# Optimization experiments

Measured on AMD Instinct MI355X. Metric: run time of the kernel, lower is better.

Reference implementation:

```python
import jax, jax.numpy as jnp
import numpy as np
from jax import lax

VOCAB, EMBED, HIDDEN, SEQ = 50257, 1024, 1024, 4096


def setup_inputs() -> dict:
    key = jax.random.key(0)
    ks = jax.random.split(key, 8)
    s = 0.02
    return {
        "input_seq": jax.random.randint(ks[0], (SEQ,), 0, VOCAB),
        "emb": jax.random.normal(ks[1], (VOCAB, EMBED), jnp.float32) * s,
        "Wrx": jax.random.normal(ks[2], (HIDDEN, EMBED), jnp.float32) * s,
        "Wrh": jax.random.normal(ks[3], (HIDDEN, HIDDEN), jnp.float32) * s,
        "Wzx": jax.random.normal(ks[4], (HIDDEN, EMBED), jnp.float32) * s,
        "Wzh": jax.random.normal(ks[5], (HIDDEN, HIDDEN), jnp.float32) * s,
        "Wx": jax.random.normal(ks[6], (HIDDEN, EMBED), jnp.float32) * s,
        "Wh": jax.random.normal(ks[7], (HIDDEN, HIDDEN), jnp.float32) * s,
    }


def reference(input_seq, emb, Wrx, Wrh, Wzx, Wzh, Wx, Wh):
    # Embed whole sequence at once: [S, E]
    x_seq = emb[input_seq]
    # Hoist input-side projections out of the recurrence (one GEMM each): [S, H]
    xr = x_seq @ Wrx.T
    xz = x_seq @ Wzx.T
    xh = x_seq @ Wx.T

    def step(h, xs):
        xr_t, xz_t, xh_t = xs
        z = jax.nn.sigmoid(xz_t + Wzh @ h)          # update gate
        r = jax.nn.sigmoid(xr_t + Wrh @ h)          # reset gate
        h_tilde = jnp.tanh(xh_t + Wh @ (r * h))     # candidate
        h_new = z * h + (1.0 - z) * h_tilde
        return h_new, None

    h0 = jnp.zeros((Wh.shape[0],), dtype=emb.dtype)
    h_final, _ = lax.scan(step, h0, (xr, xz, xh))
    return h_final
```

## Files before the change

kernel.cpp:

```cpp
#include <hip/hip_runtime.h>
#include <stdint.h>


#define HID    1024
#define SEQLEN 4096
#define NWG    64
#define RPW    16
#define BLOCK  512

typedef unsigned long long u64;

__global__ __launch_bounds__(256) void proj_gemm(
    const int* __restrict__ seq, const float* __restrict__ emb,
    const float* __restrict__ Wrx, const float* __restrict__ Wzx,
    const float* __restrict__ Wx,
    float* __restrict__ xr, float* __restrict__ xz, float* __restrict__ xh)
{
  __shared__ float As[32][68];
  __shared__ float Bs[32][68];
  __shared__ int   idx[64];

  const float* W = (blockIdx.z == 0) ? Wrx : (blockIdx.z == 1) ? Wzx : Wx;
  float*       C = (blockIdx.z == 0) ? xr  : (blockIdx.z == 1) ? xz  : xh;

  const int tid = threadIdx.x;
  const int t0 = blockIdx.y * 64;
  const int i0 = blockIdx.x * 64;
  if (tid < 64) idx[tid] = seq[t0 + tid];
  __syncthreads();

  float acc[4][4] = {};
  const int tx = tid & 15, ty = tid >> 4;
  const int c4 = (tid & 7) * 4;
  const int r8 = tid >> 3;

  for (int k0 = 0; k0 < HID; k0 += 32) {
    for (int l = 0; l < 2; ++l) {
      const int rr = r8 + l * 32;
      float4 av = *(const float4*)(emb + (size_t)idx[rr] * HID + k0 + c4);
      As[c4+0][rr]=av.x; As[c4+1][rr]=av.y; As[c4+2][rr]=av.z; As[c4+3][rr]=av.w;
      float4 bv = *(const float4*)(W + (size_t)(i0 + rr) * HID + k0 + c4);
      Bs[c4+0][rr]=bv.x; Bs[c4+1][rr]=bv.y; Bs[c4+2][rr]=bv.z; Bs[c4+3][rr]=bv.w;
    }
    __syncthreads();
    #pragma unroll
    for (int k = 0; k < 32; ++k) {
      float a[4], b[4];
      *(float4*)a = *(const float4*)&As[k][ty * 4];
      *(float4*)b = *(const float4*)&Bs[k][tx * 4];
      #pragma unroll
      for (int i = 0; i < 4; ++i)
        #pragma unroll
        for (int j = 0; j < 4; ++j)
          acc[i][j] = fmaf(a[i], b[j], acc[i][j]);
    }
    __syncthreads();
  }
  #pragma unroll
  for (int i = 0; i < 4; ++i) {
    float4 v = make_float4(acc[i][0], acc[i][1], acc[i][2], acc[i][3]);
    *(float4*)(C + (size_t)(t0 + ty * 4 + i) * HID + i0 + tx * 4) = v;
  }
}

__device__ __forceinline__ void publish2(u64* cells, int row, float a, float b,
                                         unsigned tag) {
  u64 ca = ((u64)tag << 32) | (u64)__float_as_uint(a);
  u64 cb = ((u64)tag << 32) | (u64)__float_as_uint(b);
  (void)__hip_atomic_exchange(&cells[row],     ca, __ATOMIC_RELAXED,
                              __HIP_MEMORY_SCOPE_AGENT);
  (void)__hip_atomic_exchange(&cells[row + 1], cb, __ATOMIC_RELAXED,
                              __HIP_MEMORY_SCOPE_AGENT);
}

__device__ __forceinline__ float2 poll_pair(const u64* cells, int pair,
                                            unsigned want, int* budget) {
  const float* p = (const float*)(cells + 2 * pair);
  float4 v;
  for (;;) {
    asm volatile("global_load_dwordx4 %0, %1, off sc0 sc1\n\ts_waitcnt vmcnt(0)"
                 : "=v"(v) : "v"(p) : "memory");
    if (__float_as_uint(v.y) == want && __float_as_uint(v.w) == want) break;
    if (--(*budget) <= 0) break;
  }
  return make_float2(v.x, v.z);
}

__global__ __launch_bounds__(BLOCK, 2) void rnn_scan(
    const float* __restrict__ Wzh, const float* __restrict__ Wrh,
    const float* __restrict__ Whh,
    const float* __restrict__ xz, const float* __restrict__ xr,
    const float* __restrict__ xh,
    u64* __restrict__ hcell,
    u64* __restrict__ rhcell,
    float* __restrict__ out)
{
  const int tid  = threadIdx.x;
  const int wave = tid >> 6, lane = tid & 63;
  const int g    = blockIdx.x;
  const int rowA = g * RPW + wave * 2;

  __shared__ float h_lds[HID];
  __shared__ float rh_lds[HID];

  float wgt[3][2][16];
  #pragma unroll
  for (int m = 0; m < 3; ++m) {
    const float* Wm = (m == 0) ? Wzh : (m == 1) ? Wrh : Whh;
    #pragma unroll
    for (int rr = 0; rr < 2; ++rr) {
      const float* p = Wm + (size_t)(rowA + rr) * HID + lane * 4;
      #pragma unroll
      for (int q = 0; q < 4; ++q) {
        float4 v = *(const float4*)(p + q * 256);
        wgt[m][rr][q*4+0] = v.x; wgt[m][rr][q*4+1] = v.y;
        wgt[m][rr][q*4+2] = v.z; wgt[m][rr][q*4+3] = v.w;
      }
    }
  }

  int budget = 1 << 21;
  float xzv[2], xrv[2], xhv[2], zv[2], hprev[2];

  for (int t = 1; t <= SEQLEN; ++t) {
    if (t == 1) {
      *(float2*)&h_lds[2 * tid] = make_float2(0.f, 0.f);
    } else {
      float2 hv = poll_pair(hcell + ((t - 1) & 1) * HID, tid,
                            (unsigned)(t - 1), &budget);
      *(float2*)&h_lds[2 * tid] = hv;
    }

    if (lane == 0) {
      #pragma unroll
      for (int rr = 0; rr < 2; ++rr) {
        xzv[rr] = xz[(size_t)(t - 1) * HID + rowA + rr];
        xrv[rr] = xr[(size_t)(t - 1) * HID + rowA + rr];
        xhv[rr] = xh[(size_t)(t - 1) * HID + rowA + rr];
      }
    }
    __syncthreads();

    float hr[16];
    #pragma unroll
    for (int q = 0; q < 4; ++q)
      *(float4*)&hr[q*4] = *(const float4*)&h_lds[q * 256 + lane * 4];
    float az[2] = {0.f, 0.f}, ar[2] = {0.f, 0.f};
    #pragma unroll
    for (int rr = 0; rr < 2; ++rr)
      #pragma unroll
      for (int c = 0; c < 16; ++c) {
        az[rr] = fmaf(wgt[0][rr][c], hr[c], az[rr]);
        ar[rr] = fmaf(wgt[1][rr][c], hr[c], ar[rr]);
      }
    #pragma unroll
    for (int m = 1; m < 64; m <<= 1) {
      az[0] += __shfl_xor(az[0], m, 64);
      az[1] += __shfl_xor(az[1], m, 64);
      ar[0] += __shfl_xor(ar[0], m, 64);
      ar[1] += __shfl_xor(ar[1], m, 64);
    }
    if (lane == 0) {
      float rh[2];
      #pragma unroll
      for (int rr = 0; rr < 2; ++rr) {
        hprev[rr] = h_lds[rowA + rr];
        zv[rr]    = 1.f / (1.f + __expf(-(xzv[rr] + az[rr])));
        float rg  = 1.f / (1.f + __expf(-(xrv[rr] + ar[rr])));
        rh[rr]    = rg * hprev[rr];
      }
      publish2(rhcell + (t & 1) * HID, rowA, rh[0], rh[1], (unsigned)t);
    }

    {
      float2 rv = poll_pair(rhcell + (t & 1) * HID, tid, (unsigned)t, &budget);
      *(float2*)&rh_lds[2 * tid] = rv;
    }
    __syncthreads();

    float rr16[16];
    #pragma unroll
    for (int q = 0; q < 4; ++q)
      *(float4*)&rr16[q*4] = *(const float4*)&rh_lds[q * 256 + lane * 4];
    float ac[2] = {0.f, 0.f};
    #pragma unroll
    for (int rr = 0; rr < 2; ++rr)
      #pragma unroll
      for (int c = 0; c < 16; ++c)
        ac[rr] = fmaf(wgt[2][rr][c], rr16[c], ac[rr]);
    #pragma unroll
    for (int m = 1; m < 64; m <<= 1) {
      ac[0] += __shfl_xor(ac[0], m, 64);
      ac[1] += __shfl_xor(ac[1], m, 64);
    }
    if (lane == 0) {
      float hn[2];
      #pragma unroll
      for (int rr = 0; rr < 2; ++rr) {
        float cand = tanhf(xhv[rr] + ac[rr]);
        hn[rr]     = zv[rr] * hprev[rr] + (1.f - zv[rr]) * cand;
      }
      publish2(hcell + (t & 1) * HID, rowA, hn[0], hn[1], (unsigned)t);
      if (t == SEQLEN) { out[rowA] = hn[0]; out[rowA + 1] = hn[1]; }
    }
  }
}

extern "C" void kernel_launch(void* const* d_in, const int* in_sizes, int n_in,
                              void* d_out, int out_size, void* d_ws, size_t ws_size,
                              hipStream_t stream) {
  (void)in_sizes; (void)n_in; (void)out_size; (void)ws_size;

  const int*   seq = (const int*)d_in[0];
  const float* emb = (const float*)d_in[1];
  const float* Wrx = (const float*)d_in[2];
  const float* Wrh = (const float*)d_in[3];
  const float* Wzx = (const float*)d_in[4];
  const float* Wzh = (const float*)d_in[5];
  const float* Wx  = (const float*)d_in[6];
  const float* Wh  = (const float*)d_in[7];

  char* ws = (char*)d_ws;
  const size_t PROJ = (size_t)SEQLEN * HID * sizeof(float);
  float* xr    = (float*)(ws);
  float* xz    = (float*)(ws + PROJ);
  float* xh    = (float*)(ws + 2 * PROJ);
  u64*   hcell = (u64*)(ws + 3 * PROJ);
  u64*   rhcell= hcell + 2 * HID;

  (void)hipMemsetAsync(hcell, 0xFF, 4 * HID * sizeof(u64), stream);

  proj_gemm<<<dim3(HID / 64, SEQLEN / 64, 3), 256, 0, stream>>>(
      seq, emb, Wrx, Wzx, Wx, xr, xz, xh);

  rnn_scan<<<dim3(NWG), BLOCK, 0, stream>>>(
      Wzh, Wrh, Wh, xz, xr, xh, hcell, rhcell, (float*)d_out);
}
```

Measured before the change: 24.54 ms.

## Replace per-thread tag polling with per-workgroup arrival counters; transpose projections

Each wave now bumps a padded per-workgroup counter after publishing its h or r*h values. Only wave 0 polls those 64 counters before the block does a single tag-checked gather, replacing the old scheme where all 512 threads spun on tagged cells. This is meant to cut polling traffic across the device and the latency of the cross-workgroup barrier. The projection GEMM now writes the xr/xz/xh outputs transposed (row-major per hidden unit), and their per-step loads are issued at the top of each step, ahead of the wait. The cost is extra atomics, a vmcnt wait before each counter bump, and additional block barriers per step.

```diff
diff --git a/kernel.cpp b/kernel.cpp
--- a/kernel.cpp
+++ b/kernel.cpp
@@ -7,6 +7,7 @@
 #define NWG    64
 #define RPW    16
 #define BLOCK  512
+#define SSTR   8
 
 typedef unsigned long long u64;
 
@@ -14,14 +15,14 @@
     const int* __restrict__ seq, const float* __restrict__ emb,
     const float* __restrict__ Wrx, const float* __restrict__ Wzx,
     const float* __restrict__ Wx,
-    float* __restrict__ xr, float* __restrict__ xz, float* __restrict__ xh)
+    float* __restrict__ xrT, float* __restrict__ xzT, float* __restrict__ xhT)
 {
   __shared__ float As[32][68];
   __shared__ float Bs[32][68];
   __shared__ int   idx[64];
 
   const float* W = (blockIdx.z == 0) ? Wrx : (blockIdx.z == 1) ? Wzx : Wx;
-  float*       C = (blockIdx.z == 0) ? xr  : (blockIdx.z == 1) ? xz  : xh;
+  float*       C = (blockIdx.z == 0) ? xrT : (blockIdx.z == 1) ? xzT : xhT;
 
   const int tid = threadIdx.x;
   const int t0 = blockIdx.y * 64;
@@ -46,8 +47,8 @@
     #pragma unroll
     for (int k = 0; k < 32; ++k) {
       float a[4], b[4];
-      *(float4*)a = *(const float4*)&As[k][ty * 4];
-      *(float4*)b = *(const float4*)&Bs[k][tx * 4];
+      *(float4*)a = *(const float4*)&Bs[k][ty * 4];
+      *(float4*)b = *(const float4*)&As[k][tx * 4];
       #pragma unroll
       for (int i = 0; i < 4; ++i)
         #pragma unroll
@@ -59,7 +60,7 @@
   #pragma unroll
   for (int i = 0; i < 4; ++i) {
     float4 v = make_float4(acc[i][0], acc[i][1], acc[i][2], acc[i][3]);
-    *(float4*)(C + (size_t)(t0 + ty * 4 + i) * HID + i0 + tx * 4) = v;
+    *(float4*)(C + (size_t)(i0 + ty * 4 + i) * SEQLEN + t0 + tx * 4) = v;
   }
 }
 
@@ -73,8 +74,8 @@
                               __HIP_MEMORY_SCOPE_AGENT);
 }
 
-__device__ __forceinline__ float2 poll_pair(const u64* cells, int pair,
-                                            unsigned want, int* budget) {
+__device__ __forceinline__ float2 gather_pair(const u64* cells, int pair,
+                                              unsigned want, int* budget) {
   const float* p = (const float*)(cells + 2 * pair);
   float4 v;
   for (;;) {
@@ -86,13 +87,25 @@
   return make_float2(v.x, v.z);
 }
 
+__device__ __forceinline__ void poll_sent(const u64* s, int lane, u64 need,
+                                          int* budget) {
+  const u64* p = s + (size_t)lane * SSTR;
+  for (;;) {
+    u64 v = __hip_atomic_load((u64*)p, __ATOMIC_RELAXED, __HIP_MEMORY_SCOPE_AGENT);
+    if (__all(v >= need)) break;
+    if (--(*budget) <= 0) break;
+  }
+}
+
 __global__ __launch_bounds__(BLOCK, 2) void rnn_scan(
     const float* __restrict__ Wzh, const float* __restrict__ Wrh,
     const float* __restrict__ Whh,
-    const float* __restrict__ xz, const float* __restrict__ xr,
-    const float* __restrict__ xh,
+    const float* __restrict__ xzT, const float* __restrict__ xrT,
+    const float* __restrict__ xhT,
     u64* __restrict__ hcell,
     u64* __restrict__ rhcell,
+    u64* __restrict__ sent_h,
+    u64* __restrict__ sent_rh,
     float* __restrict__ out)
 {
   const int tid  = threadIdx.x;
@@ -123,22 +136,25 @@
   float xzv[2], xrv[2], xhv[2], zv[2], hprev[2];
 
   for (int t = 1; t <= SEQLEN; ++t) {
+    if (lane == 0) {
+      #pragma unroll
+      for (int rr = 0; rr < 2; ++rr) {
+        xzv[rr] = xzT[(size_t)(rowA + rr) * SEQLEN + (t - 1)];
+        xrv[rr] = xrT[(size_t)(rowA + rr) * SEQLEN + (t - 1)];
+        xhv[rr] = xhT[(size_t)(rowA + rr) * SEQLEN + (t - 1)];
+      }
+    }
+
+    float2 hv;
     if (t == 1) {
-      *(float2*)&h_lds[2 * tid] = make_float2(0.f, 0.f);
+      hv = make_float2(0.f, 0.f);
     } else {
-      float2 hv = poll_pair(hcell + ((t - 1) & 1) * HID, tid,
-                            (unsigned)(t - 1), &budget);
-      *(float2*)&h_lds[2 * tid] = hv;
-    }
-
-    if (lane == 0) {
-      #pragma unroll
-      for (int rr = 0; rr < 2; ++rr) {
-        xzv[rr] = xz[(size_t)(t - 1) * HID + rowA + rr];
-        xrv[rr] = xr[(size_t)(t - 1) * HID + rowA + rr];
-        xhv[rr] = xh[(size_t)(t - 1) * HID + rowA + rr];
-      }
-    }
+      if (wave == 0) poll_sent(sent_h, lane, 8ull * (u64)(t - 1), &budget);
+      __syncthreads();
+      hv = gather_pair(hcell + ((t - 1) & 1) * HID, tid,
+                       (unsigned)(t - 1), &budget);
+    }
+    *(float2*)&h_lds[2 * tid] = hv;
     __syncthreads();
 
     float hr[16];
@@ -170,10 +186,15 @@
         rh[rr]    = rg * hprev[rr];
       }
       publish2(rhcell + (t & 1) * HID, rowA, rh[0], rh[1], (unsigned)t);
-    }
-
+      asm volatile("s_waitcnt vmcnt(0)" ::: "memory");
+      (void)__hip_atomic_fetch_add(&sent_rh[(size_t)g * SSTR], 1ull,
+                                   __ATOMIC_RELAXED, __HIP_MEMORY_SCOPE_AGENT);
+    }
+
+    if (wave == 0) poll_sent(sent_rh, lane, 8ull * (u64)t, &budget);
+    __syncthreads();
     {
-      float2 rv = poll_pair(rhcell + (t & 1) * HID, tid, (unsigned)t, &budget);
+      float2 rv = gather_pair(rhcell + (t & 1) * HID, tid, (unsigned)t, &budget);
       *(float2*)&rh_lds[2 * tid] = rv;
     }
     __syncthreads();
@@ -201,6 +222,9 @@
         hn[rr]     = zv[rr] * hprev[rr] + (1.f - zv[rr]) * cand;
       }
       publish2(hcell + (t & 1) * HID, rowA, hn[0], hn[1], (unsigned)t);
+      asm volatile("s_waitcnt vmcnt(0)" ::: "memory");
+      (void)__hip_atomic_fetch_add(&sent_h[(size_t)g * SSTR], 1ull,
+                                   __ATOMIC_RELAXED, __HIP_MEMORY_SCOPE_AGENT);
       if (t == SEQLEN) { out[rowA] = hn[0]; out[rowA + 1] = hn[1]; }
     }
   }
@@ -222,17 +246,21 @@
 
   char* ws = (char*)d_ws;
   const size_t PROJ = (size_t)SEQLEN * HID * sizeof(float);
-  float* xr    = (float*)(ws);
-  float* xz    = (float*)(ws + PROJ);
-  float* xh    = (float*)(ws + 2 * PROJ);
-  u64*   hcell = (u64*)(ws + 3 * PROJ);
-  u64*   rhcell= hcell + 2 * HID;
+  float* xrT    = (float*)(ws);
+  float* xzT    = (float*)(ws + PROJ);
+  float* xhT    = (float*)(ws + 2 * PROJ);
+  u64*   hcell  = (u64*)(ws + 3 * PROJ);
+  u64*   rhcell = hcell + 2 * HID;
+  u64*   sent_h = rhcell + 2 * HID;
+  u64*   sent_rh= sent_h + NWG * SSTR;
 
   (void)hipMemsetAsync(hcell, 0xFF, 4 * HID * sizeof(u64), stream);
+  (void)hipMemsetAsync(sent_h, 0x00, 2 * NWG * SSTR * sizeof(u64), stream);
 
   proj_gemm<<<dim3(HID / 64, SEQLEN / 64, 3), 256, 0, stream>>>(
-      seq, emb, Wrx, Wzx, Wx, xr, xz, xh);
+      seq, emb, Wrx, Wzx, Wx, xrT, xzT, xhT);
 
   rnn_scan<<<dim3(NWG), BLOCK, 0, stream>>>(
-      Wzh, Wrh, Wh, xz, xr, xh, hcell, rhcell, (float*)d_out);
-}
+      Wzh, Wrh, Wh, xzT, xrT, xhT, hcell, rhcell, sent_h, sent_rh,
+      (float*)d_out);
+}
```

New measurement: 31.25 ms. +27.3%, slower.

## Store input projections transposed and poll cells with 64-bit atomic loads

Applied to the files above, without the earlier changes.

The projection GEMM now writes xr/xz/xh in hidden-major (transposed) layout, so each scan workgroup reads the per-step inputs for its rows from consecutive addresses across timesteps, which should improve cache-line reuse in the serial loop. The polling routine replaces the inline-asm uncached dwordx4 load with two relaxed agent-scope 64-bit atomic loads. This may change polling latency, and the split loads could alter how visibility of the tagged cells is observed.

```diff
diff --git a/kernel.cpp b/kernel.cpp
--- a/kernel.cpp
+++ b/kernel.cpp
@@ -14,14 +14,14 @@
     const int* __restrict__ seq, const float* __restrict__ emb,
     const float* __restrict__ Wrx, const float* __restrict__ Wzx,
     const float* __restrict__ Wx,
-    float* __restrict__ xr, float* __restrict__ xz, float* __restrict__ xh)
+    float* __restrict__ xrT, float* __restrict__ xzT, float* __restrict__ xhT)
 {
   __shared__ float As[32][68];
   __shared__ float Bs[32][68];
   __shared__ int   idx[64];
 
   const float* W = (blockIdx.z == 0) ? Wrx : (blockIdx.z == 1) ? Wzx : Wx;
-  float*       C = (blockIdx.z == 0) ? xr  : (blockIdx.z == 1) ? xz  : xh;
+  float*       C = (blockIdx.z == 0) ? xrT : (blockIdx.z == 1) ? xzT : xhT;
 
   const int tid = threadIdx.x;
   const int t0 = blockIdx.y * 64;
@@ -46,8 +46,8 @@
     #pragma unroll
     for (int k = 0; k < 32; ++k) {
       float a[4], b[4];
-      *(float4*)a = *(const float4*)&As[k][ty * 4];
-      *(float4*)b = *(const float4*)&Bs[k][tx * 4];
+      *(float4*)a = *(const float4*)&Bs[k][ty * 4];
+      *(float4*)b = *(const float4*)&As[k][tx * 4];
       #pragma unroll
       for (int i = 0; i < 4; ++i)
         #pragma unroll
@@ -59,7 +59,7 @@
   #pragma unroll
   for (int i = 0; i < 4; ++i) {
     float4 v = make_float4(acc[i][0], acc[i][1], acc[i][2], acc[i][3]);
-    *(float4*)(C + (size_t)(t0 + ty * 4 + i) * HID + i0 + tx * 4) = v;
+    *(float4*)(C + (size_t)(i0 + ty * 4 + i) * SEQLEN + t0 + tx * 4) = v;
   }
 }
 
@@ -75,22 +75,25 @@
 
 __device__ __forceinline__ float2 poll_pair(const u64* cells, int pair,
                                             unsigned want, int* budget) {
-  const float* p = (const float*)(cells + 2 * pair);
-  float4 v;
+  const u64* p = cells + 2 * pair;
+  u64 c0, c1;
   for (;;) {
-    asm volatile("global_load_dwordx4 %0, %1, off sc0 sc1\n\ts_waitcnt vmcnt(0)"
-                 : "=v"(v) : "v"(p) : "memory");
-    if (__float_as_uint(v.y) == want && __float_as_uint(v.w) == want) break;
+    c0 = __hip_atomic_load((u64*)(p + 0), __ATOMIC_RELAXED,
+                           __HIP_MEMORY_SCOPE_AGENT);
+    c1 = __hip_atomic_load((u64*)(p + 1), __ATOMIC_RELAXED,
+                           __HIP_MEMORY_SCOPE_AGENT);
+    if ((unsigned)(c0 >> 32) == want && (unsigned)(c1 >> 32) == want) break;
     if (--(*budget) <= 0) break;
   }
-  return make_float2(v.x, v.z);
+  return make_float2(__uint_as_float((unsigned)c0),
+                     __uint_as_float((unsigned)c1));
 }
 
 __global__ __launch_bounds__(BLOCK, 2) void rnn_scan(
     const float* __restrict__ Wzh, const float* __restrict__ Wrh,
     const float* __restrict__ Whh,
-    const float* __restrict__ xz, const float* __restrict__ xr,
-    const float* __restrict__ xh,
+    const float* __restrict__ xzT, const float* __restrict__ xrT,
+    const float* __restrict__ xhT,
     u64* __restrict__ hcell,
     u64* __restrict__ rhcell,
     float* __restrict__ out)
@@ -134,9 +137,9 @@
     if (lane == 0) {
       #pragma unroll
       for (int rr = 0; rr < 2; ++rr) {
-        xzv[rr] = xz[(size_t)(t - 1) * HID + rowA + rr];
-        xrv[rr] = xr[(size_t)(t - 1) * HID + rowA + rr];
-        xhv[rr] = xh[(size_t)(t - 1) * HID + rowA + rr];
+        xzv[rr] = xzT[(size_t)(rowA + rr) * SEQLEN + (t - 1)];
+        xrv[rr] = xrT[(size_t)(rowA + rr) * SEQLEN + (t - 1)];
+        xhv[rr] = xhT[(size_t)(rowA + rr) * SEQLEN + (t - 1)];
       }
     }
     __syncthreads();
@@ -222,17 +225,17 @@
 
   char* ws = (char*)d_ws;
   const size_t PROJ = (size_t)SEQLEN * HID * sizeof(float);
-  float* xr    = (float*)(ws);
-  float* xz    = (float*)(ws + PROJ);
-  float* xh    = (float*)(ws + 2 * PROJ);
-  u64*   hcell = (u64*)(ws + 3 * PROJ);
-  u64*   rhcell= hcell + 2 * HID;
+  float* xrT    = (float*)(ws);
+  float* xzT    = (float*)(ws + PROJ);
+  float* xhT    = (float*)(ws + 2 * PROJ);
+  u64*   hcell  = (u64*)(ws + 3 * PROJ);
+  u64*   rhcell = hcell + 2 * HID;
 
   (void)hipMemsetAsync(hcell, 0xFF, 4 * HID * sizeof(u64), stream);
 
   proj_gemm<<<dim3(HID / 64, SEQLEN / 64, 3), 256, 0, stream>>>(
-      seq, emb, Wrx, Wzx, Wx, xr, xz, xh);
+      seq, emb, Wrx, Wzx, Wx, xrT, xzT, xhT);
 
   rnn_scan<<<dim3(NWG), BLOCK, 0, stream>>>(
-      Wzh, Wrh, Wh, xz, xr, xh, hcell, rhcell, (float*)d_out);
-}
+      Wzh, Wrh, Wh, xzT, xrT, xhT, hcell, rhcell, (float*)d_out);
+}
```

Measured after the change: 29.70 ms. 1.21x slower.
